# Optimization experiments

Measured on AMD Instinct MI355X. Metric: run time of the kernel, lower is better.

## Reference

```python
import jax, jax.numpy as jnp
import numpy as np

B, K, HID, EMB = 16384, 8, 512, 512


def setup_inputs() -> dict:
    key = jax.random.key(0)
    ks = jax.random.split(key, 6)
    scale = 1.0 / np.sqrt(HID)
    return {
        "query": jax.random.normal(ks[0], (B, HID), jnp.float32),
        "topics": jax.random.normal(ks[1], (B, K, EMB), jnp.float32),
        "coverage_vector": jax.random.uniform(ks[2], (B, K), jnp.float32),
        "Ua_w": jax.random.normal(ks[3], (HID, EMB), jnp.float32) * scale,
        "Wa_w": jax.random.normal(ks[4], (HID, HID), jnp.float32) * scale,
        "va_w": jax.random.normal(ks[5], (HID,), jnp.float32) * scale,
        "va_b": jnp.zeros((1,), jnp.float32),
    }


def reference(query, topics, coverage_vector, Ua_w, Wa_w, va_w, va_b):
    # Faithful to the torch loop: query is re-projected by Wa EACH step,
    # so step i uses Wa^(i+1)(query) -- a sequential recurrence over K topics.
    # proj_key for all topics can be batched: [B,K,EMB] @ Ua_w.T -> [B,K,HID]
    proj_key = jnp.einsum('bke,he->bkh', topics, Ua_w)

    def step(q, pk_i):
        # q: [B,HID]; pk_i: [B,HID] (proj_key for topic i)
        q_new = q @ Wa_w.T
        s = jnp.tanh(q_new + pk_i) @ va_w + va_b[0]  # [B]
        return q_new, s

    # scan over the K topic steps (carry = evolving query)
    _, scores = jax.lax.scan(step, query, jnp.moveaxis(proj_key, 1, 0))
    scores = scores.T * coverage_vector  # [B,K]
    alphas = jax.nn.softmax(scores, axis=1)
    mt = jnp.einsum('bk,bke->be', alphas, topics)
    return mt, alphas
```

## Files before the change

kernel.cpp:

```cpp
#include <hip/hip_runtime.h>
#include <hip/hip_bf16.h>

#define HID 512
#define EMB 512
#define KTOP 8
#define BM 64
#define THREADS 1024
#define POWN (512 * 512)

typedef __attribute__((ext_vector_type(8))) short bf16x8;
typedef __attribute__((ext_vector_type(4))) float f32x4;
typedef __attribute__((ext_vector_type(4))) unsigned u32x4;

__device__ __forceinline__ short f2bf(float f) {
    unsigned u = __builtin_bit_cast(unsigned, f);
    u += 0x7fffu + ((u >> 16) & 1u);
    return (short)(u >> 16);
}
__device__ __forceinline__ float bf2f(short s) {
    unsigned u = ((unsigned)(unsigned short)s) << 16;
    return __builtin_bit_cast(float, u);
}
__device__ __forceinline__ unsigned cvtpk2(float x, float y) {
    return ((unsigned)(unsigned short)f2bf(x)) |
           (((unsigned)(unsigned short)f2bf(y)) << 16);
}
__device__ __forceinline__ bf16x8 pack8(f32x4 a, f32x4 b) {
    u32x4 r = {cvtpk2(a[0], a[1]), cvtpk2(a[2], a[3]),
               cvtpk2(b[0], b[1]), cvtpk2(b[2], b[3])};
    return __builtin_bit_cast(bf16x8, r);
}
__device__ __forceinline__ void split_bf(float w, short& hi, short& lo) {
    hi = f2bf(w);
    lo = f2bf(w - bf2f(hi));
}

__global__ void prep_kernel(const float* __restrict__ Wa, const float* __restrict__ Ua,
                            short* __restrict__ hiRM, short* __restrict__ loRM,
                            short* __restrict__ hiT, short* __restrict__ loT,
                            short* __restrict__ ua_b) {
    int i = blockIdx.x * blockDim.x + threadIdx.x;
    if (i >= POWN) return;
    int r = i >> 9, c = i & 511;
    short hi, lo;
    split_bf(Wa[i], hi, lo);
    hiRM[i] = hi; loRM[i] = lo;
    hiT[c * 512 + r] = hi;
    loT[c * 512 + r] = lo;
    ua_b[i] = f2bf(Ua[i]);
}

__device__ __forceinline__ int sel4(int4 v, int i) {
    int r = v.x;
    if (i == 1) r = v.y;
    if (i == 2) r = v.z;
    if (i == 3) r = v.w;
    return r;
}

__global__ __launch_bounds__(256)
void powmul_kernel(short* __restrict__ hiRM, short* __restrict__ loRM,
                   short* __restrict__ hiT, short* __restrict__ loT,
                   int4 aS, int4 bS, int4 dS) {
    const int p = blockIdx.z;
    const int as = sel4(aS, p), bs = sel4(bS, p), ds = sel4(dS, p);
    const short* Ah = hiRM + (size_t)as * POWN;
    const short* Al = loRM + (size_t)as * POWN;
    const short* Bh = hiT + (size_t)bs * POWN;
    const short* Bl = loT + (size_t)bs * POWN;

    const int tid = threadIdx.x, lane = tid & 63, w = tid >> 6;
    const int l15 = lane & 15, lg = lane >> 4;
    const int row = blockIdx.x * 64 + w * 16 + l15;
    const int colb = blockIdx.y * 64;

    f32x4 acc[4];
#pragma unroll
    for (int nf = 0; nf < 4; ++nf) acc[nf] = (f32x4){0.f, 0.f, 0.f, 0.f};

    for (int ch = 0; ch < 16; ++ch) {
        const int e0 = ch * 32 + lg * 8;
        bf16x8 ah = *(const bf16x8*)(Ah + row * 512 + e0);
        bf16x8 al = *(const bf16x8*)(Al + row * 512 + e0);
#pragma unroll
        for (int nf = 0; nf < 4; ++nf) {
            const int col = colb + nf * 16 + l15;
            bf16x8 bh = *(const bf16x8*)(Bh + col * 512 + e0);
            bf16x8 bl = *(const bf16x8*)(Bl + col * 512 + e0);
            acc[nf] = __builtin_amdgcn_mfma_f32_16x16x32_bf16(ah, bh, acc[nf], 0, 0, 0);
            acc[nf] = __builtin_amdgcn_mfma_f32_16x16x32_bf16(ah, bl, acc[nf], 0, 0, 0);
            acc[nf] = __builtin_amdgcn_mfma_f32_16x16x32_bf16(al, bh, acc[nf], 0, 0, 0);
        }
    }

    short* Dh = hiRM + (size_t)ds * POWN;
    short* Dl = loRM + (size_t)ds * POWN;
#pragma unroll
    for (int nf = 0; nf < 4; ++nf)
#pragma unroll
        for (int j = 0; j < 4; ++j) {
            int rg = blockIdx.x * 64 + w * 16 + lg * 4 + j;
            int cg = colb + nf * 16 + l15;
            short hi, lo;
            split_bf(acc[nf][j], hi, lo);
            Dh[rg * 512 + cg] = hi;
            Dl[rg * 512 + cg] = lo;
            if (ds < 4) {
                hiT[(size_t)ds * POWN + cg * 512 + rg] = hi;
                loT[(size_t)ds * POWN + cg * 512 + rg] = lo;
            }
        }
}

__global__ __launch_bounds__(256)
void swz_pow_kernel(const short* __restrict__ pow_hi, const short* __restrict__ pow_lo,
                    const short* __restrict__ ua_b,
                    short* __restrict__ swz_hi, short* __restrict__ swz_lo,
                    short* __restrict__ swz_ua) {
    const int m = blockIdx.y;
    const short* src;
    short* dst;
    if (m < 8)       { src = pow_hi + (size_t)m * POWN;       dst = swz_hi + (size_t)m * POWN; }
    else if (m < 16) { src = pow_lo + (size_t)(m - 8) * POWN; dst = swz_lo + (size_t)(m - 8) * POWN; }
    else             { src = ua_b;                             dst = swz_ua; }

#pragma unroll
    for (int i = 0; i < 8; ++i) {
        int c = blockIdx.x * 2048 + i * 256 + threadIdx.x;
        bf16x8 v = *(const bf16x8*)(src + c * 8);
        int ch = (c >> 2) & 15;
        int lg = c & 3;
        int cb = c >> 10;
        int l15 = (c >> 6) & 15;
        int lane = lg * 16 + l15;
        *(bf16x8*)(dst + ((size_t)(ch * 32 + cb) * 64 + lane) * 8) = v;
    }
}

__global__ __launch_bounds__(THREADS)
void q_prep_kernel(const float* __restrict__ query, short* __restrict__ q_sw) {
    __shared__ short q_s[BM * 512];
    const int tid = threadIdx.x;
    const long rbase = (long)blockIdx.x * BM;

#pragma unroll
    for (int i = 0; i < 4; ++i) {
        int idx = tid + i * THREADS;
        int r = idx >> 6, s = idx & 63;
        const float* qp = query + (rbase + r) * HID + s * 8;
        f32x4 a = *(const f32x4*)qp;
        f32x4 b = *(const f32x4*)(qp + 4);
        *(bf16x8*)&q_s[(r * 64 + (s ^ (r & 7))) * 8] = pack8(a, b);
    }
    __syncthreads();
    short* dst = q_sw + (size_t)blockIdx.x * (BM * 512);
#pragma unroll
    for (int i = 0; i < 4; ++i) {
        int d = tid + i * THREADS;
        int l15 = d & 15, lg = (d >> 4) & 3;
        int ch = (d >> 6) & 15, mf = (d >> 10) & 3;
        int r = mf * 16 + l15;
        int s = ch * 4 + lg;
        bf16x8 v = *(const bf16x8*)&q_s[(r * 64 + (s ^ (r & 7))) * 8];
        *(bf16x8*)(dst + (size_t)d * 8) = v;
    }
}

__global__ __launch_bounds__(THREADS, 4)
void attn_main_kernel(const float* __restrict__ topics,
                      const float* __restrict__ cov,
                      const short* __restrict__ q_sw,
                      const short* __restrict__ swz_hi,
                      const short* __restrict__ swz_lo,
                      const short* __restrict__ swz_ua,
                      const float* __restrict__ va_w,
                      const float* __restrict__ va_b,
                      float* __restrict__ out_mt,
                      float* __restrict__ out_alpha) {
    __shared__ short t_lds[BM * 512];
    __shared__ float scores_s[BM][KTOP];
    __shared__ float alpha_s[BM][KTOP];

    const int tid  = threadIdx.x;
    const int lane = tid & 63;
    const int wn   = tid >> 6;
    const int l15  = lane & 15;
    const int lg   = lane >> 4;
    const long rbase = (long)blockIdx.x * BM;

    if (tid < BM * KTOP) ((float*)scores_s)[tid] = 0.f;

    float va_reg[2];
#pragma unroll
    for (int nf = 0; nf < 2; ++nf) va_reg[nf] = va_w[wn * 32 + nf * 16 + l15];
    const float vab = va_b[0];

    const short* qbase = q_sw + (size_t)blockIdx.x * (BM * 512) + lane * 8;
    const int lane8 = lane * 8;

#pragma unroll 1
    for (int step = 0; step < KTOP; ++step) {
        __syncthreads();
#pragma unroll
        for (int i = 0; i < 4; ++i) {
            int idx = tid + i * THREADS;
            int r = idx >> 6, s = idx & 63;
            const float* tp = topics + ((rbase + r) * KTOP + step) * EMB + s * 8;
            f32x4 a = *(const f32x4*)tp;
            f32x4 b = *(const f32x4*)(tp + 4);
            *(bf16x8*)&t_lds[(r * 64 + (s ^ (r & 7))) * 8] = pack8(a, b);
        }
        __syncthreads();

        const short* wh = swz_hi + (size_t)step * POWN;
        const short* wl = swz_lo + (size_t)step * POWN;

        f32x4 acc[4][2];
#pragma unroll
        for (int mf = 0; mf < 4; ++mf)
#pragma unroll
            for (int nf = 0; nf < 2; ++nf) acc[mf][nf] = (f32x4){0.f, 0.f, 0.f, 0.f};

        for (int ch = 0; ch < 16; ++ch) {
            bf16x8 qf[4], tf[4];
#pragma unroll
            for (int mf = 0; mf < 4; ++mf) {
                qf[mf] = *(const bf16x8*)(qbase + (size_t)(mf * 16 + ch) * 512);
                int r = mf * 16 + l15;
                int s = ch * 4 + lg;
                tf[mf] = *(const bf16x8*)&t_lds[(r * 64 + (s ^ (r & 7))) * 8];
            }
#pragma unroll
            for (int nf = 0; nf < 2; ++nf) {
                const size_t off = (size_t)((ch * 32 + wn * 2 + nf) * 512 + lane8);
                bf16x8 bh = *(const bf16x8*)(wh + off);
                bf16x8 bl = *(const bf16x8*)(wl + off);
                bf16x8 bu = *(const bf16x8*)(swz_ua + off);
#pragma unroll
                for (int mf = 0; mf < 4; ++mf) {
                    acc[mf][nf] = __builtin_amdgcn_mfma_f32_16x16x32_bf16(qf[mf], bh, acc[mf][nf], 0, 0, 0);
                    acc[mf][nf] = __builtin_amdgcn_mfma_f32_16x16x32_bf16(qf[mf], bl, acc[mf][nf], 0, 0, 0);
                    acc[mf][nf] = __builtin_amdgcn_mfma_f32_16x16x32_bf16(tf[mf], bu, acc[mf][nf], 0, 0, 0);
                }
            }
        }

        float part[4][4];
#pragma unroll
        for (int mf = 0; mf < 4; ++mf)
#pragma unroll
            for (int j = 0; j < 4; ++j) part[mf][j] = 0.f;
#pragma unroll
        for (int mf = 0; mf < 4; ++mf)
#pragma unroll
            for (int nf = 0; nf < 2; ++nf)
#pragma unroll
                for (int j = 0; j < 4; ++j) {
                    float x = acc[mf][nf][j];
                    float e = __expf(2.f * x);
                    float th = 1.f - 2.f / (e + 1.f);
                    part[mf][j] += th * va_reg[nf];
                }
#pragma unroll
        for (int m = 8; m >= 1; m >>= 1)
#pragma unroll
            for (int mf = 0; mf < 4; ++mf)
#pragma unroll
                for (int j = 0; j < 4; ++j)
                    part[mf][j] += __shfl_xor(part[mf][j], m, 64);
        if (l15 == 0) {
#pragma unroll
            for (int mf = 0; mf < 4; ++mf)
#pragma unroll
                for (int j = 0; j < 4; ++j)
                    atomicAdd(&scores_s[mf * 16 + lg * 4 + j][step], part[mf][j]);
        }
    }

    __syncthreads();
    if (tid < BM * KTOP) {
        int r = tid >> 3, k = tid & 7;
        scores_s[r][k] = (scores_s[r][k] + vab) * cov[(rbase + r) * KTOP + k];
    }
    __syncthreads();
    if (tid < BM) {
        float mx = scores_s[tid][0];
#pragma unroll
        for (int k = 1; k < KTOP; ++k) mx = fmaxf(mx, scores_s[tid][k]);
        float e[KTOP], sum = 0.f;
#pragma unroll
        for (int k = 0; k < KTOP; ++k) { e[k] = __expf(scores_s[tid][k] - mx); sum += e[k]; }
#pragma unroll
        for (int k = 0; k < KTOP; ++k) {
            float a = e[k] / sum;
            alpha_s[tid][k] = a;
            out_alpha[(rbase + tid) * KTOP + k] = a;
        }
    }
    __syncthreads();

#pragma unroll 1
    for (int i = tid; i < BM * (EMB / 4); i += THREADS) {
        int r = i >> 7;
        int c4 = i & 127;
        const float* tb = topics + (rbase + r) * KTOP * EMB + c4 * 4;
        f32x4 acc = {0.f, 0.f, 0.f, 0.f};
#pragma unroll
        for (int k = 0; k < KTOP; ++k) {
            f32x4 t = *(const f32x4*)(tb + k * EMB);
            float a = alpha_s[r][k];
            acc[0] += t[0] * a;
            acc[1] += t[1] * a;
            acc[2] += t[2] * a;
            acc[3] += t[3] * a;
        }
        *(f32x4*)(out_mt + (rbase + r) * EMB + c4 * 4) = acc;
    }
}

extern "C" void kernel_launch(void* const* d_in, const int* in_sizes, int n_in,
                              void* d_out, int out_size, void* d_ws, size_t ws_size,
                              hipStream_t stream) {
    const float* query  = (const float*)d_in[0];
    const float* topics = (const float*)d_in[1];
    const float* cov    = (const float*)d_in[2];
    const float* Ua     = (const float*)d_in[3];
    const float* Wa     = (const float*)d_in[4];
    const float* va     = (const float*)d_in[5];
    const float* vab    = (const float*)d_in[6];

    const int Brows = in_sizes[0] / HID;
    const int nblk  = Brows / BM;

    short* pow_hi = (short*)d_ws;
    short* pow_lo = pow_hi + (size_t)8 * POWN;
    short* hiT    = pow_lo + (size_t)8 * POWN;
    short* loT    = hiT + (size_t)4 * POWN;
    short* ua_b   = loT + (size_t)4 * POWN;
    short* swz_hi = ua_b + POWN;
    short* swz_lo = swz_hi + (size_t)8 * POWN;
    short* swz_ua = swz_lo + (size_t)8 * POWN;
    short* q_sw   = swz_ua + POWN;

    float* out_mt    = (float*)d_out;
    float* out_alpha = out_mt + (size_t)Brows * EMB;

    prep_kernel<<<(POWN + 255) / 256, 256, 0, stream>>>(Wa, Ua, pow_hi, pow_lo,
                                                        hiT, loT, ua_b);
    powmul_kernel<<<dim3(8, 8, 1), 256, 0, stream>>>(pow_hi, pow_lo, hiT, loT,
        make_int4(0, 0, 0, 0), make_int4(0, 0, 0, 0), make_int4(1, 0, 0, 0));
    powmul_kernel<<<dim3(8, 8, 2), 256, 0, stream>>>(pow_hi, pow_lo, hiT, loT,
        make_int4(1, 1, 0, 0), make_int4(0, 1, 0, 0), make_int4(2, 3, 0, 0));
    powmul_kernel<<<dim3(8, 8, 4), 256, 0, stream>>>(pow_hi, pow_lo, hiT, loT,
        make_int4(3, 3, 2, 3), make_int4(0, 1, 3, 3), make_int4(4, 5, 6, 7));

    swz_pow_kernel<<<dim3(16, 17), 256, 0, stream>>>(pow_hi, pow_lo, ua_b,
                                                     swz_hi, swz_lo, swz_ua);
    q_prep_kernel<<<nblk, THREADS, 0, stream>>>(query, q_sw);

    attn_main_kernel<<<nblk, THREADS, 0, stream>>>(topics, cov, q_sw,
                                                   swz_hi, swz_lo, swz_ua,
                                                   va, vab, out_mt, out_alpha);
}
```

Baseline: 401.3 us.

## Double-buffer topic tiles, swizzle block order, split mt into separate kernel

The main kernel now double-buffers the bf16 topic tile in LDS, loading step+1 while step's MFMAs run, which removes one barrier per step. Block indices are remapped so neighbouring blocks take strided row groups, and the weighted-sum output mt moves into its own streaming kernel that reads alphas from global memory. The aim is to hide global-load latency behind compute and shorten the tail of the main kernel. The cost is twice the LDS (64KB for topics), which can lower occupancy, plus an extra launch that reads topics again.

```diff
diff --git a/kernel.cpp b/kernel.cpp
--- a/kernel.cpp
+++ b/kernel.cpp
@@ -175,18 +175,18 @@
                       const short* __restrict__ swz_ua,
                       const float* __restrict__ va_w,
                       const float* __restrict__ va_b,
-                      float* __restrict__ out_mt,
                       float* __restrict__ out_alpha) {
-    __shared__ short t_lds[BM * 512];
+    __shared__ short t_lds[2][BM * 512];
     __shared__ float scores_s[BM][KTOP];
-    __shared__ float alpha_s[BM][KTOP];
 
     const int tid  = threadIdx.x;
     const int lane = tid & 63;
     const int wn   = tid >> 6;
     const int l15  = lane & 15;
     const int lg   = lane >> 4;
-    const long rbase = (long)blockIdx.x * BM;
+    const int bid  = blockIdx.x;
+    const int blk  = (bid & 7) * (int)(gridDim.x >> 3) + (bid >> 3);
+    const long rbase = (long)blk * BM;
 
     if (tid < BM * KTOP) ((float*)scores_s)[tid] = 0.f;
 
@@ -195,22 +195,35 @@
     for (int nf = 0; nf < 2; ++nf) va_reg[nf] = va_w[wn * 32 + nf * 16 + l15];
     const float vab = va_b[0];
 
-    const short* qbase = q_sw + (size_t)blockIdx.x * (BM * 512) + lane * 8;
+    const short* qbase = q_sw + (size_t)blk * (BM * 512) + lane * 8;
     const int lane8 = lane * 8;
+
+#pragma unroll
+    for (int i = 0; i < 4; ++i) {
+        int idx = tid + i * THREADS;
+        int r = idx >> 6, s = idx & 63;
+        const float* tp = topics + ((rbase + r) * KTOP + 0) * EMB + s * 8;
+        f32x4 a = *(const f32x4*)tp;
+        f32x4 b = *(const f32x4*)(tp + 4);
+        *(bf16x8*)&t_lds[0][(r * 64 + (s ^ (r & 7))) * 8] = pack8(a, b);
+    }
+    __syncthreads();
 
 #pragma unroll 1
     for (int step = 0; step < KTOP; ++step) {
-        __syncthreads();
-#pragma unroll
-        for (int i = 0; i < 4; ++i) {
-            int idx = tid + i * THREADS;
-            int r = idx >> 6, s = idx & 63;
-            const float* tp = topics + ((rbase + r) * KTOP + step) * EMB + s * 8;
-            f32x4 a = *(const f32x4*)tp;
-            f32x4 b = *(const f32x4*)(tp + 4);
-            *(bf16x8*)&t_lds[(r * 64 + (s ^ (r & 7))) * 8] = pack8(a, b);
-        }
-        __syncthreads();
+        const int cur = step & 1;
+
+        if (step < KTOP - 1) {
+#pragma unroll
+            for (int i = 0; i < 4; ++i) {
+                int idx = tid + i * THREADS;
+                int r = idx >> 6, s = idx & 63;
+                const float* tp = topics + ((rbase + r) * KTOP + (step + 1)) * EMB + s * 8;
+                f32x4 a = *(const f32x4*)tp;
+                f32x4 b = *(const f32x4*)(tp + 4);
+                *(bf16x8*)&t_lds[cur ^ 1][(r * 64 + (s ^ (r & 7))) * 8] = pack8(a, b);
+            }
+        }
 
         const short* wh = swz_hi + (size_t)step * POWN;
         const short* wl = swz_lo + (size_t)step * POWN;
@@ -228,12 +241,12 @@
                 qf[mf] = *(const bf16x8*)(qbase + (size_t)(mf * 16 + ch) * 512);
                 int r = mf * 16 + l15;
                 int s = ch * 4 + lg;
-                tf[mf] = *(const bf16x8*)&t_lds[(r * 64 + (s ^ (r & 7))) * 8];
+                tf[mf] = *(const bf16x8*)&t_lds[cur][(r * 64 + (s ^ (r & 7))) * 8];
             }
 #pragma unroll
             for (int nf = 0; nf < 2; ++nf) {
                 const size_t off = (size_t)((ch * 32 + wn * 2 + nf) * 512 + lane8);
-                bf16x8 bh = *(const bf16x8*)(wh + off);
+                bf16x8 bh = *(const bf16x8*)(swz_hi + (size_t)step * POWN + off);
                 bf16x8 bl = *(const bf16x8*)(wl + off);
                 bf16x8 bu = *(const bf16x8*)(swz_ua + off);
 #pragma unroll
@@ -244,6 +257,7 @@
                 }
             }
         }
+        (void)wh;
 
         float part[4][4];
 #pragma unroll
@@ -275,9 +289,10 @@
                 for (int j = 0; j < 4; ++j)
                     atomicAdd(&scores_s[mf * 16 + lg * 4 + j][step], part[mf][j]);
         }
-    }
-
-    __syncthreads();
+
+        __syncthreads();
+    }
+
     if (tid < BM * KTOP) {
         int r = tid >> 3, k = tid & 7;
         scores_s[r][k] = (scores_s[r][k] + vab) * cov[(rbase + r) * KTOP + k];
@@ -291,31 +306,37 @@
 #pragma unroll
         for (int k = 0; k < KTOP; ++k) { e[k] = __expf(scores_s[tid][k] - mx); sum += e[k]; }
 #pragma unroll
-        for (int k = 0; k < KTOP; ++k) {
-            float a = e[k] / sum;
-            alpha_s[tid][k] = a;
-            out_alpha[(rbase + tid) * KTOP + k] = a;
-        }
-    }
-    __syncthreads();
-
-#pragma unroll 1
-    for (int i = tid; i < BM * (EMB / 4); i += THREADS) {
-        int r = i >> 7;
-        int c4 = i & 127;
-        const float* tb = topics + (rbase + r) * KTOP * EMB + c4 * 4;
-        f32x4 acc = {0.f, 0.f, 0.f, 0.f};
-#pragma unroll
-        for (int k = 0; k < KTOP; ++k) {
-            f32x4 t = *(const f32x4*)(tb + k * EMB);
-            float a = alpha_s[r][k];
-            acc[0] += t[0] * a;
-            acc[1] += t[1] * a;
-            acc[2] += t[2] * a;
-            acc[3] += t[3] * a;
-        }
-        *(f32x4*)(out_mt + (rbase + r) * EMB + c4 * 4) = acc;
-    }
+        for (int k = 0; k < KTOP; ++k)
+            out_alpha[(rbase + tid) * KTOP + k] = e[k] / sum;
+    }
+}
+
+__global__ __launch_bounds__(256)
+void mt_kernel(const float* __restrict__ topics, const float* __restrict__ alphas,
+               float* __restrict__ out_mt) {
+    int idx = blockIdx.x * 256 + threadIdx.x;
+    int r  = idx >> 5;
+    int c0 = (idx & 31) * 16;
+    float a[KTOP];
+#pragma unroll
+    for (int k = 0; k < KTOP; ++k) a[k] = alphas[(size_t)r * KTOP + k];
+    const float* tb = topics + (size_t)r * KTOP * EMB + c0;
+    f32x4 o[4];
+#pragma unroll
+    for (int u = 0; u < 4; ++u) o[u] = (f32x4){0.f, 0.f, 0.f, 0.f};
+#pragma unroll
+    for (int k = 0; k < KTOP; ++k)
+#pragma unroll
+        for (int u = 0; u < 4; ++u) {
+            f32x4 t = *(const f32x4*)(tb + k * EMB + u * 4);
+            o[u][0] += a[k] * t[0];
+            o[u][1] += a[k] * t[1];
+            o[u][2] += a[k] * t[2];
+            o[u][3] += a[k] * t[3];
+        }
+    float* mp = out_mt + (size_t)r * EMB + c0;
+#pragma unroll
+    for (int u = 0; u < 4; ++u) *(f32x4*)(mp + u * 4) = o[u];
 }
 
 extern "C" void kernel_launch(void* const* d_in, const int* in_sizes, int n_in,
@@ -360,5 +381,6 @@
 
     attn_main_kernel<<<nblk, THREADS, 0, stream>>>(topics, cov, q_sw,
                                                    swz_hi, swz_lo, swz_ua,
-                                                   va, vab, out_mt, out_alpha);
-}
+                                                   va, vab, out_alpha);
+    mt_kernel<<<(Brows * EMB / 16) / 256, 256, 0, stream>>>(topics, out_alpha, out_mt);
+}
```

Measured after the change: 458.3 us. 14.2% more time.
